# Optimization experiments

Hardware: AMD Instinct MI355X
Metric: run time of the kernel (lower is better)

The kernel has to match this reference:

```python
import jax, jax.numpy as jnp
import numpy as np

B, S, H = 4, 8192, 768
E, K = 8, 2


def setup_inputs() -> dict:
    key = jax.random.key(0)
    ks = jax.random.split(key, 5)
    scale = 1.0 / np.sqrt(H)
    x = jax.random.normal(ks[0], (B, S, H), dtype=jnp.float32)
    router_w = jax.random.uniform(ks[1], (E, H), jnp.float32, -scale, scale)   # torch Linear(h, E).weight
    router_b = jax.random.uniform(ks[2], (E,), jnp.float32, -scale, scale)
    expert_w = jax.random.uniform(ks[3], (E, H, H), jnp.float32, -scale, scale)  # [E, out, in]
    expert_b = jax.random.uniform(ks[4], (E, H), jnp.float32, -scale, scale)
    return {"x": x, "router_w": router_w, "router_b": router_b,
            "expert_w": expert_w, "expert_b": expert_b}


def reference(x, router_w, router_b, expert_w, expert_b):
    # Router: scores [b,s,E] -> softmax -> top-k probs/ids
    scores = jnp.einsum('bsh,eh->bse', x, router_w) + router_b
    probs = jax.nn.softmax(scores, axis=-1)
    top_probs, expert_ids = jax.lax.top_k(probs, K)          # [b,s,K]
    # Dense grouped expert linears: y[b,s,e,d] = x[b,s,:] @ W_e.T + b_e
    y = jnp.einsum('bsh,edh->bsed', x, expert_w) + expert_b   # [b,s,E,H]
    # Gather the k selected experts' outputs per token
    out_k = jnp.take_along_axis(y, expert_ids[..., None], axis=2)  # [b,s,K,H]
    # Normalize top-k probs and combine
    w = top_probs / (jnp.sum(top_probs, axis=-1, keepdims=True) + 1e-9)  # [b,s,K]
    out = jnp.einsum('bsk,bskh->bsh', w, out_k)
    return out
```

## Files before the change

### kernel.cpp

```cpp
#include <hip/hip_runtime.h>
#include <stdint.h>

#define TOK 32768
#define H 768
#define NE 8
#define CAP 8192
#define BM 128
#define BN 128
#define BK 32

typedef __bf16 bf16x8 __attribute__((ext_vector_type(8)));
typedef float  f32x4  __attribute__((ext_vector_type(4)));

#define OFF_ASSIGN 256
#define OFF_L0 (OFF_ASSIGN + TOK*16)
#define OFF_W0 (OFF_L0 + NE*CAP*4)
#define OFF_L1 (OFF_W0 + NE*CAP*4)
#define OFF_W1 (OFF_L1 + NE*CAP*4)
#define OFF_XB (OFF_W1 + NE*CAP*4)
#define OFF_WB (OFF_XB + (size_t)TOK*H*2)

__device__ __forceinline__ unsigned short f2bf(float f) {
    uint32_t u = __builtin_bit_cast(uint32_t, f);
    u = (u + 0x7fffu + ((u >> 16) & 1u)) >> 16;
    return (unsigned short)u;
}

__device__ __forceinline__ void async_cp16(const void* g, void* l) {
    __builtin_amdgcn_global_load_lds(
        (const __attribute__((address_space(1))) void*)g,
        (__attribute__((address_space(3))) void*)l, 16, 0, 0);
}

__global__ __launch_bounds__(256) void convert_w(const float* __restrict__ src,
                                                 unsigned short* __restrict__ dst, int n4) {
    int i = blockIdx.x * 256 + threadIdx.x;
    if (i < n4) {
        float4 v = ((const float4*)src)[i];
        ushort4 h;
        h.x = f2bf(v.x); h.y = f2bf(v.y); h.z = f2bf(v.z); h.w = f2bf(v.w);
        ((ushort4*)dst)[i] = h;
    }
}

__global__ __launch_bounds__(256) void router_kernel(
    const float* __restrict__ x, const float* __restrict__ rw, const float* __restrict__ rb,
    unsigned short* __restrict__ xb, int4* __restrict__ assign)
{
    int wid  = threadIdx.x >> 6;
    int lane = threadIdx.x & 63;
    int token = blockIdx.x * 4 + wid;

    const float4* xr  = (const float4*)(x + (size_t)token * H);
    const float4* rw4 = (const float4*)rw;

    float s[NE];
    #pragma unroll
    for (int e = 0; e < NE; e++) s[e] = 0.f;

    #pragma unroll
    for (int i = 0; i < 3; i++) {
        int p = lane + 64 * i;
        float4 xv = xr[p];
        ushort4 xh;
        xh.x = f2bf(xv.x); xh.y = f2bf(xv.y); xh.z = f2bf(xv.z); xh.w = f2bf(xv.w);
        ((ushort4*)(xb + (size_t)token * H))[p] = xh;
        #pragma unroll
        for (int e = 0; e < NE; e++) {
            float4 wv = rw4[e * 192 + p];
            s[e] += xv.x * wv.x + xv.y * wv.y + xv.z * wv.z + xv.w * wv.w;
        }
    }
    #pragma unroll
    for (int e = 0; e < NE; e++) {
        float v = s[e];
        #pragma unroll
        for (int off = 32; off; off >>= 1) v += __shfl_xor(v, off, 64);
        s[e] = v + rb[e];
    }
    if (lane == 0) {
        int e0 = 0;
        #pragma unroll
        for (int e = 1; e < NE; e++) if (s[e] > s[e0]) e0 = e;
        int e1 = -1;
        #pragma unroll
        for (int e = 0; e < NE; e++) {
            if (e == e0) continue;
            if (e1 < 0 || s[e] > s[e1]) e1 = e;
        }
        float mx = s[e0];
        float Z = 0.f;
        #pragma unroll
        for (int e = 0; e < NE; e++) Z += __expf(s[e] - mx);
        float p0 = __expf(s[e0] - mx) / Z;
        float p1 = __expf(s[e1] - mx) / Z;
        float inv = 1.f / (p0 + p1 + 1e-9f);
        int4 a;
        a.x = e0; a.y = e1;
        a.z = __float_as_int(p0 * inv);
        a.w = __float_as_int(p1 * inv);
        assign[token] = a;
    }
}

#define SCAT_T 1024
__global__ __launch_bounds__(256) void scatter_kernel(
    const int4* __restrict__ assign, int* __restrict__ counts,
    int* __restrict__ l0, float* __restrict__ w0,
    int* __restrict__ l1, float* __restrict__ w1)
{
    __shared__ int lcnt[2 * NE];
    __shared__ int lbase[2 * NE];
    int tid = threadIdx.x;
    if (tid < 2 * NE) lcnt[tid] = 0;
    __syncthreads();

    int4 a[SCAT_T / 256];
    int  r0[SCAT_T / 256], r1[SCAT_T / 256];
    #pragma unroll
    for (int j = 0; j < SCAT_T / 256; j++) {
        int token = blockIdx.x * SCAT_T + j * 256 + tid;
        a[j] = assign[token];
        r0[j] = atomicAdd(&lcnt[a[j].x], 1);
        r1[j] = atomicAdd(&lcnt[NE + a[j].y], 1);
    }
    __syncthreads();
    if (tid < 2 * NE) lbase[tid] = atomicAdd(&counts[tid], lcnt[tid]);
    __syncthreads();

    #pragma unroll
    for (int j = 0; j < SCAT_T / 256; j++) {
        int token = blockIdx.x * SCAT_T + j * 256 + tid;
        int p0 = lbase[a[j].x] + r0[j];
        int p1 = lbase[NE + a[j].y] + r1[j];
        l0[a[j].x * CAP + p0] = token; w0[a[j].x * CAP + p0] = __int_as_float(a[j].z);
        l1[a[j].y * CAP + p1] = token; w1[a[j].y * CAP + p1] = __int_as_float(a[j].w);
    }
}

template <bool ACCUM>
__global__ __launch_bounds__(256) void expert_gemm(
    const unsigned short* __restrict__ xb, const unsigned short* __restrict__ wb,
    const float* __restrict__ eb, const int* __restrict__ counts,
    const int* __restrict__ lists, const float* __restrict__ wlists,
    float* __restrict__ out)
{
    int e   = blockIdx.z;
    int cnt = counts[e];
    int m0  = blockIdx.x * BM;
    if (m0 >= cnt) return;
    int n0  = blockIdx.y * BN;

    __shared__ unsigned short As[BM][BK];
    __shared__ unsigned short Bs[BN][BK];
    __shared__ int   toks[BM];
    __shared__ float wts[BM];

    int tid = threadIdx.x;
    if (tid < BM) {
        int g = m0 + tid;
        int t = 0; float w = 0.f;
        if (g < cnt) { t = lists[e * CAP + g]; w = wlists[e * CAP + g]; }
        toks[tid] = t; wts[tid] = w;
    }
    __syncthreads();

    int wid = tid >> 6, lane = tid & 63;
    int wm = wid & 1, wn = wid >> 1;
    int quad = lane >> 4, r16 = lane & 15;

    int srow = wid * 16 + (lane >> 2);
    int c8   = (lane & 3) * 8;
    int rA0 = srow, rA1 = 64 + srow;

    const unsigned short* srcA0 = xb + (size_t)toks[rA0] * H + c8;
    const unsigned short* srcA1 = xb + (size_t)toks[rA1] * H + c8;
    const unsigned short* srcB0 = wb + ((size_t)e * H + n0 + rA0) * H + c8;
    const unsigned short* srcB1 = wb + ((size_t)e * H + n0 + rA1) * H + c8;
    char* dstA0 = (char*)&As[0][0] + wid * 1024;
    char* dstA1 = dstA0 + 4096;
    char* dstB0 = (char*)&Bs[0][0] + wid * 1024;
    char* dstB1 = dstB0 + 4096;

    f32x4 acc[4][4] = {};

    for (int k0 = 0; k0 < H; k0 += BK) {
        async_cp16(srcA0 + k0, dstA0);
        async_cp16(srcA1 + k0, dstA1);
        async_cp16(srcB0 + k0, dstB0);
        async_cp16(srcB1 + k0, dstB1);
        __syncthreads();

        bf16x8 a[4], b[4];
        #pragma unroll
        for (int mi = 0; mi < 4; mi++)
            a[mi] = *(const bf16x8*)&As[wm * 64 + mi * 16 + r16][quad * 8];
        #pragma unroll
        for (int ni = 0; ni < 4; ni++)
            b[ni] = *(const bf16x8*)&Bs[wn * 64 + ni * 16 + r16][quad * 8];

        #pragma unroll
        for (int mi = 0; mi < 4; mi++)
            #pragma unroll
            for (int ni = 0; ni < 4; ni++)
                acc[mi][ni] = __builtin_amdgcn_mfma_f32_16x16x32_bf16(a[mi], b[ni], acc[mi][ni], 0, 0, 0);
        __syncthreads();
    }

    float bias[4];
    #pragma unroll
    for (int ni = 0; ni < 4; ni++)
        bias[ni] = eb[e * H + n0 + wn * 64 + ni * 16 + r16];

    #pragma unroll
    for (int mi = 0; mi < 4; mi++) {
        int rowb = wm * 64 + mi * 16 + quad * 4;
        #pragma unroll
        for (int r = 0; r < 4; r++) {
            int row = rowb + r;
            if (m0 + row < cnt) {
                float w = wts[row];
                float* orow = out + (size_t)toks[row] * H + n0 + wn * 64;
                #pragma unroll
                for (int ni = 0; ni < 4; ni++) {
                    float v = (acc[mi][ni][r] + bias[ni]) * w;
                    if (ACCUM) v += orow[ni * 16 + r16];
                    orow[ni * 16 + r16] = v;
                }
            }
        }
    }
}

extern "C" void kernel_launch(void* const* d_in, const int* in_sizes, int n_in,
                              void* d_out, int out_size, void* d_ws, size_t ws_size,
                              hipStream_t stream) {
    const float* x   = (const float*)d_in[0];
    const float* rw  = (const float*)d_in[1];
    const float* rb  = (const float*)d_in[2];
    const float* ew  = (const float*)d_in[3];
    const float* ebv = (const float*)d_in[4];
    float* out = (float*)d_out;

    char* ws = (char*)d_ws;
    int*   counts = (int*)ws;
    int4*  assign = (int4*)(ws + OFF_ASSIGN);
    int*   l0     = (int*)(ws + OFF_L0);
    float* w0     = (float*)(ws + OFF_W0);
    int*   l1     = (int*)(ws + OFF_L1);
    float* w1     = (float*)(ws + OFF_W1);
    unsigned short* xb = (unsigned short*)(ws + OFF_XB);
    unsigned short* wb = (unsigned short*)(ws + OFF_WB);

    hipMemsetAsync(counts, 0, 64, stream);

    int n4 = NE * H * H / 4;
    convert_w<<<(n4 + 255) / 256, 256, 0, stream>>>(ew, wb, n4);
    router_kernel<<<TOK / 4, 256, 0, stream>>>(x, rw, rb, xb, assign);
    scatter_kernel<<<TOK / SCAT_T, 256, 0, stream>>>(assign, counts, l0, w0, l1, w1);

    dim3 grid(CAP / BM, H / BN, NE);
    expert_gemm<false><<<grid, 256, 0, stream>>>(xb, wb, ebv, counts,      l0, w0, out);
    expert_gemm<true ><<<grid, 256, 0, stream>>>(xb, wb, ebv, counts + NE, l1, w1, out);
}
```

Measured before the change: 366.1 us.

## Triple-buffer expert GEMM LDS tiles with async prefetch two stages ahead

The expert GEMM main loop now uses three LDS buffers per operand, prefetching tile t+2 with global_load_lds while computing tile t. A vmcnt wait plus a barrier replaces the two full syncthreads per iteration. The LDS layout is also changed to a fragment-major order, so each lane reads its MFMA operand as one contiguous 16-byte chunk, which avoids bank conflicts. The cost is three times the LDS use, which may limit occupancy, and some redundant final-tile loads at the end of the loop.

```diff
diff --git a/kernel.cpp b/kernel.cpp
--- a/kernel.cpp
+++ b/kernel.cpp
@@ -151,8 +151,8 @@
     if (m0 >= cnt) return;
     int n0  = blockIdx.y * BN;
 
-    __shared__ unsigned short As[BM][BK];
-    __shared__ unsigned short Bs[BN][BK];
+    __shared__ unsigned short As[3][BM * BK];
+    __shared__ unsigned short Bs[3][BN * BK];
     __shared__ int   toks[BM];
     __shared__ float wts[BM];
 
@@ -169,43 +169,54 @@
     int wm = wid & 1, wn = wid >> 1;
     int quad = lane >> 4, r16 = lane & 15;
 
-    int srow = wid * 16 + (lane >> 2);
-    int c8   = (lane & 3) * 8;
-    int rA0 = srow, rA1 = 64 + srow;
-
-    const unsigned short* srcA0 = xb + (size_t)toks[rA0] * H + c8;
-    const unsigned short* srcA1 = xb + (size_t)toks[rA1] * H + c8;
-    const unsigned short* srcB0 = wb + ((size_t)e * H + n0 + rA0) * H + c8;
-    const unsigned short* srcB1 = wb + ((size_t)e * H + n0 + rA1) * H + c8;
-    char* dstA0 = (char*)&As[0][0] + wid * 1024;
-    char* dstA1 = dstA0 + 4096;
-    char* dstB0 = (char*)&Bs[0][0] + wid * 1024;
-    char* dstB1 = dstB0 + 4096;
+    int frow = wid * 16 + r16;
+    int c8   = quad * 8;
+
+    const unsigned short* gA0 = xb + (size_t)toks[frow]      * H + c8;
+    const unsigned short* gA1 = xb + (size_t)toks[64 + frow] * H + c8;
+    const unsigned short* gB0 = wb + ((size_t)e * H + n0 + frow)      * H + c8;
+    const unsigned short* gB1 = wb + ((size_t)e * H + n0 + 64 + frow) * H + c8;
+    char* dA = (char*)&As[0][0] + wid * 1024;
+    char* dB = (char*)&Bs[0][0] + wid * 1024;
 
     f32x4 acc[4][4] = {};
 
-    for (int k0 = 0; k0 < H; k0 += BK) {
-        async_cp16(srcA0 + k0, dstA0);
-        async_cp16(srcA1 + k0, dstA1);
-        async_cp16(srcB0 + k0, dstB0);
-        async_cp16(srcB1 + k0, dstB1);
-        __syncthreads();
-
+#define STAGE(buf, kel) do { int _bo = (buf) * 8192;      \
+    async_cp16(gA0 + (kel), dA + _bo);                    \
+    async_cp16(gA1 + (kel), dA + _bo + 4096);             \
+    async_cp16(gB0 + (kel), dB + _bo);                    \
+    async_cp16(gB1 + (kel), dB + _bo + 4096); } while (0)
+
+    constexpr int NT = H / BK;
+    STAGE(0, 0);
+    STAGE(1, BK);
+    asm volatile("s_waitcnt vmcnt(4)" ::: "memory");
+    __builtin_amdgcn_s_barrier();
+
+    for (int t = 0; t < NT; t++) {
+        int tn = (t + 2 < NT) ? (t + 2) : (NT - 1);
+        STAGE((t + 2) % 3, tn * BK);
+
+        const unsigned short* Ac = &As[t % 3][0];
+        const unsigned short* Bc = &Bs[t % 3][0];
         bf16x8 a[4], b[4];
         #pragma unroll
         for (int mi = 0; mi < 4; mi++)
-            a[mi] = *(const bf16x8*)&As[wm * 64 + mi * 16 + r16][quad * 8];
+            a[mi] = *(const bf16x8*)(Ac + (wm * 4 + mi) * 512 + lane * 8);
         #pragma unroll
         for (int ni = 0; ni < 4; ni++)
-            b[ni] = *(const bf16x8*)&Bs[wn * 64 + ni * 16 + r16][quad * 8];
+            b[ni] = *(const bf16x8*)(Bc + (wn * 4 + ni) * 512 + lane * 8);
 
         #pragma unroll
         for (int mi = 0; mi < 4; mi++)
             #pragma unroll
             for (int ni = 0; ni < 4; ni++)
                 acc[mi][ni] = __builtin_amdgcn_mfma_f32_16x16x32_bf16(a[mi], b[ni], acc[mi][ni], 0, 0, 0);
-        __syncthreads();
-    }
+
+        asm volatile("s_waitcnt vmcnt(4)" ::: "memory");
+        __builtin_amdgcn_s_barrier();
+    }
+#undef STAGE
 
     float bias[4];
     #pragma unroll
```

New measurement: 464.1 us. 1.27x slower.
